# Kernel optimization log

Measured on AMD Instinct MI355X. Metric: run time of the kernel, lower is better.

## Reference

```python
import jax, jax.numpy as jnp
import numpy as np

NEG_INF = -9.0e15  # matches torch's -9000000000000000.0 mask value
ALPHA = 0.2        # LeakyReLU negative slope from init_kwargs


def setup_inputs() -> dict:
    key = jax.random.key(0)
    k1, k2, k3, k4, k5 = jax.random.split(key, 5)
    B, N, D, A = 64, 128, 128, 1000
    hidden = jax.random.normal(k1, (B, N, D), dtype=jnp.float32)
    adj = jax.random.randint(k2, (B, N, N), 0, 5)  # edge types 0..4 (0 = masked)
    a = jax.random.normal(k3, (D, 4), dtype=jnp.float32) * 0.1  # stacked a_0..a_3
    A_attr_sess = jax.random.uniform(k4, (B, N, A), dtype=jnp.float32)
    attr_embedding = jax.random.normal(k5, (A, D), dtype=jnp.float32)
    return {"hidden": hidden, "adj": adj, "a": a,
            "A_attr_sess": A_attr_sess, "attr_embedding": attr_embedding}


def reference(hidden, adj, a, A_attr_sess, attr_embedding):
    # a_input[b,i,j,:] = leaky_relu(h[b,i,:] * h[b,j,:])  -> [B,N,N,D]
    a_input = jax.nn.leaky_relu(hidden[:, :, None, :] * hidden[:, None, :, :],
                                negative_slope=ALPHA)
    # four edge-type scores in one contraction: [B,N,N,4]
    e = jnp.einsum('bijd,dk->bijk', a_input, a)
    # masked selection by adjacency edge type (later writes override earlier)
    alpha = jnp.full(adj.shape, NEG_INF, dtype=e.dtype)
    alpha = jnp.where(adj == 1, e[..., 0], alpha)
    alpha = jnp.where(adj == 2, e[..., 1], alpha)
    alpha = jnp.where(adj == 3, e[..., 2], alpha)
    alpha = jnp.where(adj == 4, e[..., 3], alpha)
    attn = jax.nn.softmax(alpha, axis=-1)        # [B,N,N]
    output = jnp.einsum('bij,bjd->bid', attn, hidden)  # [B,N,D]
    attr_sess = jnp.einsum('bna,ad->bnd', A_attr_sess, attr_embedding)
    return output, attr_sess
```

## Files before the change

kernel.cpp:

```cpp
#include <hip/hip_runtime.h>

#define BB 64
#define NN 128
#define DD 128
#define AA 1000
#define KPAD 1024
#define NEG_INF (-9.0e15f)

typedef __attribute__((ext_vector_type(8))) short short8;
typedef __attribute__((ext_vector_type(4))) float floatx4;
typedef __attribute__((ext_vector_type(4))) unsigned int uintx4;
typedef __attribute__((ext_vector_type(2))) unsigned int uintx2;

__device__ __forceinline__ float bflo(unsigned int u) { return __uint_as_float(u << 16); }
__device__ __forceinline__ float bfhi(unsigned int u) { return __uint_as_float(u & 0xffff0000u); }
__device__ __forceinline__ unsigned int packbf(float f0, float f1) {
  return (__float_as_uint(f0) >> 16) | (__float_as_uint(f1) & 0xffff0000u);
}
__device__ __forceinline__ unsigned short bf_rne(float f) {
  unsigned int u = __float_as_uint(f);
  return (unsigned short)((u + 0x7fffu + ((u >> 16) & 1u)) >> 16);
}
__device__ __forceinline__ unsigned int packbf_rne(float f0, float f1) {
  return (unsigned int)bf_rne(f0) | ((unsigned int)bf_rne(f1) << 16);
}
__device__ __forceinline__ short8 u2s(uintx4 v) {
  union { uintx4 u; short8 s; } x; x.u = v; return x.s;
}

__global__ __launch_bounds__(256) void prep_kernel(
    const float* __restrict__ hidden, const float* __restrict__ emb,
    unsigned short* __restrict__ ET, unsigned short* __restrict__ HTg)
{
  const int t = threadIdx.x;
  const int bid = blockIdx.x;
  if (bid < BB) {
    __shared__ float hsf[NN * 129];
    const float* hb = hidden + (size_t)bid * NN * DD;
    #pragma unroll
    for (int u = 0; u < 16; ++u) {
      int e = u * 1024 + t * 4;
      float4 v = *reinterpret_cast<const float4*>(hb + e);
      int r = e >> 7, c = e & 127;
      float* d = &hsf[r * 129 + c];
      d[0] = v.x; d[1] = v.y; d[2] = v.z; d[3] = v.w;
    }
    __syncthreads();
    unsigned short* ht16 = HTg + (size_t)bid * NN * DD;
    #pragma unroll
    for (int u = 0; u < 8; ++u) {
      int e = u * 2048 + t * 8;
      int dI = e >> 7, il = e & 127;
      float x[8];
      #pragma unroll
      for (int j = 0; j < 8; ++j) x[j] = hsf[(il + j) * 129 + dI];
      uintx4 o;
      o.x = packbf_rne(x[0], x[1]); o.y = packbf_rne(x[2], x[3]);
      o.z = packbf_rne(x[4], x[5]); o.w = packbf_rne(x[6], x[7]);
      *reinterpret_cast<uintx4*>(ht16 + e) = o;
    }
  } else {
    int c = bid - BB;
    int k0 = t * 4;
    float x[4];
    #pragma unroll
    for (int j = 0; j < 4; ++j) {
      int k = k0 + j;
      x[j] = (k < AA) ? emb[(size_t)k * DD + c] : 0.f;
    }
    uintx2 o;
    o.x = packbf_rne(x[0], x[1]);
    o.y = packbf_rne(x[2], x[3]);
    *reinterpret_cast<uintx2*>(ET + (size_t)c * KPAD + k0) = o;
  }
}

struct AttnSmem {
  __align__(16) unsigned short Hs[NN * 128];
  union {
    __align__(16) unsigned short As[4 * 16 * 256];
    struct {
      __align__(16) float Sa[16 * 129];
      __align__(16) unsigned short W[16 * 128];
    } sw;
  } u2;
  __align__(16) float saf[4 * 256];
};

#define BK 64
struct AttrSmem {
  __align__(16) unsigned short ETs[2][DD * BK];
  __align__(16) unsigned short As2[2][32 * BK];
};

union FusedSmem { AttnSmem a; AttrSmem g; };

__device__ __forceinline__ void attn_body(
    AttnSmem& s, const float* __restrict__ hidden,
    const int* __restrict__ adj, const float* __restrict__ amat,
    const unsigned short* __restrict__ HTg, float* __restrict__ out0)
{
  const int t = threadIdx.x;
  const int L = t & 63, w = t >> 6;
  const int lr = L & 15, lq = L >> 4;
  const int b = blockIdx.x >> 3;
  const int i0 = (blockIdx.x & 7) * 16;

  const int* adjb = adj + ((size_t)b * NN + i0) * NN;
  int adjv[8];
  #pragma unroll
  for (int nt = 0; nt < 2; ++nt)
    #pragma unroll
    for (int r = 0; r < 4; ++r)
      adjv[nt * 4 + r] = adjb[(lq * 4 + r) * NN + w * 32 + nt * 16 + lr];

  const float* hb = hidden + (size_t)b * NN * DD;
  #pragma unroll
  for (int u = 0; u < 8; ++u) {
    int id = u * 256 + t;
    int r = id >> 4, c = id & 15;
    const float* src = hb + r * 128 + c * 8;
    float4 v0 = *reinterpret_cast<const float4*>(src);
    float4 v1 = *reinterpret_cast<const float4*>(src + 4);
    uintx4 o;
    o.x = packbf_rne(v0.x, v0.y); o.y = packbf_rne(v0.z, v0.w);
    o.z = packbf_rne(v1.x, v1.y); o.w = packbf_rne(v1.z, v1.w);
    *reinterpret_cast<uintx4*>(&s.Hs[r * 128 + ((c ^ (r & 15)) << 3)]) = o;
  }
  {
    float v1 = amat[t], v2 = amat[t + 256];
    int dI = t >> 2, k = t & 3;
    s.saf[k * 256 + dI] = 0.6f * v1;
    s.saf[k * 256 + 128 + dI] = 0.4f * v1;
    s.saf[k * 256 + 64 + dI] = 0.6f * v2;
    s.saf[k * 256 + 192 + dI] = 0.4f * v2;
  }
  __syncthreads();

  #pragma unroll
  for (int u = 0; u < 8; ++u) {
    int id = u * 256 + t;
    int k = id >> 9, ii = (id >> 5) & 15, c = id & 31;
    int srow = i0 + ii;
    int dchunk = c & 15;
    uintx4 hv = *reinterpret_cast<const uintx4*>(
        &s.Hs[srow * 128 + ((dchunk ^ (srow & 15)) << 3)]);
    if (c & 16) {
      hv.x &= 0x7fff7fffu; hv.y &= 0x7fff7fffu;
      hv.z &= 0x7fff7fffu; hv.w &= 0x7fff7fffu;
    }
    const float* sf = &s.saf[k * 256 + c * 8];
    uintx4 o;
    o.x = packbf(bflo(hv.x) * sf[0], bfhi(hv.x) * sf[1]);
    o.y = packbf(bflo(hv.y) * sf[2], bfhi(hv.y) * sf[3]);
    o.z = packbf(bflo(hv.z) * sf[4], bfhi(hv.z) * sf[5]);
    o.w = packbf(bflo(hv.w) * sf[6], bfhi(hv.w) * sf[7]);
    *reinterpret_cast<uintx4*>(&s.u2.As[k * 4096 + ii * 256 + ((c ^ ii) << 3)]) = o;
  }
  __syncthreads();

  floatx4 acc[4][2];
  #pragma unroll
  for (int k = 0; k < 4; ++k)
    #pragma unroll
    for (int nt = 0; nt < 2; ++nt) acc[k][nt] = floatx4{0.f, 0.f, 0.f, 0.f};

  #pragma unroll
  for (int kt = 0; kt < 8; ++kt) {
    int ca = lq + 4 * kt;
    short8 afr[4];
    #pragma unroll
    for (int k = 0; k < 4; ++k)
      afr[k] = *reinterpret_cast<const short8*>(
          &s.u2.As[k * 4096 + lr * 256 + ((ca ^ lr) << 3)]);
    int cb = lq + 4 * (kt & 3);
    short8 bfr[2];
    #pragma unroll
    for (int nt = 0; nt < 2; ++nt) {
      int jrow = w * 32 + nt * 16 + lr;
      uintx4 hv = *reinterpret_cast<const uintx4*>(
          &s.Hs[jrow * 128 + ((cb ^ (jrow & 15)) << 3)]);
      if (kt >= 4) {
        hv.x &= 0x7fff7fffu; hv.y &= 0x7fff7fffu;
        hv.z &= 0x7fff7fffu; hv.w &= 0x7fff7fffu;
      }
      bfr[nt] = u2s(hv);
    }
    #pragma unroll
    for (int k = 0; k < 4; ++k)
      #pragma unroll
      for (int nt = 0; nt < 2; ++nt)
        acc[k][nt] = __builtin_amdgcn_mfma_f32_16x16x32_bf16(
            afr[k], bfr[nt], acc[k][nt], 0, 0, 0);
  }
  __syncthreads();

  short8 pvb[2][4];
  const unsigned short* ht = HTg + (size_t)b * NN * DD;
  #pragma unroll
  for (int nt = 0; nt < 2; ++nt)
    #pragma unroll
    for (int kt = 0; kt < 4; ++kt) {
      int dI = w * 32 + nt * 16 + lr;
      pvb[nt][kt] = *reinterpret_cast<const short8*>(ht + dI * 128 + kt * 32 + lq * 8);
    }

  #pragma unroll
  for (int nt = 0; nt < 2; ++nt)
    #pragma unroll
    for (int r = 0; r < 4; ++r) {
      int ii = lq * 4 + r;
      int j = w * 32 + nt * 16 + lr;
      int ad = adjv[nt * 4 + r];
      float al = NEG_INF;
      al = (ad == 1) ? acc[0][nt][r] : al;
      al = (ad == 2) ? acc[1][nt][r] : al;
      al = (ad == 3) ? acc[2][nt][r] : al;
      al = (ad == 4) ? acc[3][nt][r] : al;
      s.u2.sw.Sa[ii * 129 + j] = al;
    }
  __syncthreads();

  #pragma unroll
  for (int p = 0; p < 4; ++p) {
    int ii = w * 4 + p;
    float a1 = s.u2.sw.Sa[ii * 129 + L];
    float a2 = s.u2.sw.Sa[ii * 129 + 64 + L];
    float m = fmaxf(a1, a2);
    #pragma unroll
    for (int off = 32; off > 0; off >>= 1) m = fmaxf(m, __shfl_xor(m, off, 64));
    float e1 = __expf(fmaxf(a1 - m, -80.f));
    float e2 = __expf(fmaxf(a2 - m, -80.f));
    float ss = e1 + e2;
    #pragma unroll
    for (int off = 32; off > 0; off >>= 1) ss += __shfl_xor(ss, off, 64);
    float inv = 1.f / ss;
    int j2 = L + 64;
    s.u2.sw.W[ii * 128 + (((L >> 3) ^ ii) << 3) + (L & 7)] = bf_rne(e1 * inv);
    s.u2.sw.W[ii * 128 + (((j2 >> 3) ^ ii) << 3) + (j2 & 7)] = bf_rne(e2 * inv);
  }
  __syncthreads();

  floatx4 oacc[2];
  oacc[0] = floatx4{0.f, 0.f, 0.f, 0.f};
  oacc[1] = floatx4{0.f, 0.f, 0.f, 0.f};
  #pragma unroll
  for (int kt = 0; kt < 4; ++kt) {
    int c = lq + 4 * kt;
    short8 wf = *reinterpret_cast<const short8*>(
        &s.u2.sw.W[lr * 128 + ((c ^ lr) << 3)]);
    #pragma unroll
    for (int nt = 0; nt < 2; ++nt)
      oacc[nt] = __builtin_amdgcn_mfma_f32_16x16x32_bf16(
          wf, pvb[nt][kt], oacc[nt], 0, 0, 0);
  }
  float* ob = out0 + ((size_t)b * NN + i0) * DD;
  #pragma unroll
  for (int nt = 0; nt < 2; ++nt)
    #pragma unroll
    for (int r = 0; r < 4; ++r)
      ob[(lq * 4 + r) * DD + w * 32 + nt * 16 + lr] = oacc[nt][r];
}

__device__ __forceinline__ void attr_body(
    AttrSmem& s, const float* __restrict__ Aattr,
    const unsigned short* __restrict__ ET, float* __restrict__ out1)
{
  const int t = threadIdx.x;
  const int L = t & 63, w = t >> 6;
  const int lr = L & 15, lq = L >> 4;
  const int r0 = (blockIdx.x - 512) * 32;

  float4 pa0, pa1;
  uintx4 pe[4];
  const int ar = t >> 3, ak = (t & 7) * 8;
  const int ec = t >> 1, ej0 = (t & 1) * 4;

  auto fetch = [&](int it) {
    int kb = it * BK;
    int k4 = kb + ak;
    float4 z = {0.f, 0.f, 0.f, 0.f};
    pa0 = (k4 < AA) ? *reinterpret_cast<const float4*>(Aattr + (size_t)(r0 + ar) * AA + k4) : z;
    pa1 = (k4 + 4 < AA) ? *reinterpret_cast<const float4*>(Aattr + (size_t)(r0 + ar) * AA + k4 + 4) : z;
    #pragma unroll
    for (int q = 0; q < 4; ++q)
      pe[q] = *reinterpret_cast<const uintx4*>(ET + (size_t)ec * KPAD + kb + (ej0 + q) * 8);
  };
  auto stage = [&](int buf) {
    uintx4 o;
    o.x = packbf(pa0.x, pa0.y); o.y = packbf(pa0.z, pa0.w);
    o.z = packbf(pa1.x, pa1.y); o.w = packbf(pa1.z, pa1.w);
    int ac = t & 7;
    *reinterpret_cast<uintx4*>(&s.As2[buf][ar * BK + ((ac ^ (ar & 7)) << 3)]) = o;
    #pragma unroll
    for (int q = 0; q < 4; ++q)
      *reinterpret_cast<uintx4*>(&s.ETs[buf][ec * BK + (((ej0 + q) ^ (ec & 7)) << 3)]) = pe[q];
  };

  floatx4 acc[2][2];
  #pragma unroll
  for (int mt = 0; mt < 2; ++mt)
    #pragma unroll
    for (int nt = 0; nt < 2; ++nt) acc[mt][nt] = floatx4{0.f, 0.f, 0.f, 0.f};

  fetch(0);
  for (int it = 0; it < 16; ++it) {
    stage(it & 1);
    __syncthreads();
    if (it < 15) fetch(it + 1);
    #pragma unroll
    for (int ks = 0; ks < 2; ++ks) {
      int c = lq + 4 * ks;
      short8 af[2], bf[2];
      #pragma unroll
      for (int mt = 0; mt < 2; ++mt) {
        int row = mt * 16 + lr;
        af[mt] = *reinterpret_cast<const short8*>(
            &s.As2[it & 1][row * BK + ((c ^ (row & 7)) << 3)]);
      }
      #pragma unroll
      for (int nt = 0; nt < 2; ++nt) {
        int n = w * 32 + nt * 16 + lr;
        bf[nt] = *reinterpret_cast<const short8*>(
            &s.ETs[it & 1][n * BK + ((c ^ (n & 7)) << 3)]);
      }
      #pragma unroll
      for (int mt = 0; mt < 2; ++mt)
        #pragma unroll
        for (int nt = 0; nt < 2; ++nt)
          acc[mt][nt] = __builtin_amdgcn_mfma_f32_16x16x32_bf16(
              af[mt], bf[nt], acc[mt][nt], 0, 0, 0);
    }
  }

  float* ob = out1 + (size_t)r0 * DD;
  #pragma unroll
  for (int mt = 0; mt < 2; ++mt)
    #pragma unroll
    for (int nt = 0; nt < 2; ++nt)
      #pragma unroll
      for (int r = 0; r < 4; ++r)
        ob[(mt * 16 + lq * 4 + r) * DD + w * 32 + nt * 16 + lr] = acc[mt][nt][r];
}

__global__ __launch_bounds__(256, 3) void fused_kernel(
    const float* __restrict__ hidden, const int* __restrict__ adj,
    const float* __restrict__ amat, const float* __restrict__ Aattr,
    const unsigned short* __restrict__ ET, const unsigned short* __restrict__ HTg,
    float* __restrict__ out0, float* __restrict__ out1)
{
  __shared__ FusedSmem sm;
  if (blockIdx.x < 512) attn_body(sm.a, hidden, adj, amat, HTg, out0);
  else                  attr_body(sm.g, Aattr, ET, out1);
}

extern "C" void kernel_launch(void* const* d_in, const int* in_sizes, int n_in,
                              void* d_out, int out_size, void* d_ws, size_t ws_size,
                              hipStream_t stream) {
  const float* hidden = (const float*)d_in[0];
  const int*   adj    = (const int*)d_in[1];
  const float* amat   = (const float*)d_in[2];
  const float* Aattr  = (const float*)d_in[3];
  const float* emb    = (const float*)d_in[4];

  float* out0 = (float*)d_out;
  float* out1 = out0 + (size_t)BB * NN * DD;

  unsigned short* ET  = (unsigned short*)d_ws;
  unsigned short* HTg = ET + (size_t)DD * KPAD;

  prep_kernel<<<BB + DD, 256, 0, stream>>>(hidden, emb, ET, HTg);
  fused_kernel<<<768, 256, 0, stream>>>(hidden, adj, amat, Aattr, ET, HTg,
                                        out0, out1);
}
```

Measured before the change: 105.7 us.

## Pair attention and attribute GEMM work per block, coalesce embedding transpose

The fused kernel now launches 512 blocks, and each block does one 16-row attention tile plus one 16-row attribute-GEMM tile. Even and odd blocks run the two phases in opposite order so memory-heavy and compute-heavy phases are mixed across the GPU, and block indices are remapped. The attribute GEMM tile shrinks to 16 rows with an unrolled double buffer, and launch bounds change from 3 to 2 blocks per SM. The embedding transpose in the prep kernel now goes through shared memory with coalesced loads and runs in 32 blocks instead of 128. The cost is less parallelism per block phase and lower occupancy.

Result: no change. 104.4 us, median of 2 (-1.2%).

```diff
diff --git a/kernel.cpp b/kernel.cpp
--- a/kernel.cpp
+++ b/kernel.cpp
@@ -32,10 +32,10 @@
     const float* __restrict__ hidden, const float* __restrict__ emb,
     unsigned short* __restrict__ ET, unsigned short* __restrict__ HTg)
 {
+  __shared__ float hsf[NN * 129];
   const int t = threadIdx.x;
   const int bid = blockIdx.x;
   if (bid < BB) {
-    __shared__ float hsf[NN * 129];
     const float* hb = hidden + (size_t)bid * NN * DD;
     #pragma unroll
     for (int u = 0; u < 16; ++u) {
@@ -60,18 +60,30 @@
       *reinterpret_cast<uintx4*>(ht16 + e) = o;
     }
   } else {
-    int c = bid - BB;
-    int k0 = t * 4;
-    float x[4];
-    #pragma unroll
-    for (int j = 0; j < 4; ++j) {
-      int k = k0 + j;
-      x[j] = (k < AA) ? emb[(size_t)k * DD + c] : 0.f;
-    }
-    uintx2 o;
-    o.x = packbf_rne(x[0], x[1]);
-    o.y = packbf_rne(x[2], x[3]);
-    *reinterpret_cast<uintx2*>(ET + (size_t)c * KPAD + k0) = o;
+    const int k0 = (bid - BB) * 32;
+    #pragma unroll
+    for (int u = 0; u < 4; ++u) {
+      int e = u * 1024 + t * 4;
+      int r = e >> 7, c = e & 127;
+      float4 z = {0.f, 0.f, 0.f, 0.f};
+      float4 v = (k0 + r < AA)
+          ? *reinterpret_cast<const float4*>(emb + (size_t)(k0 + r) * DD + c) : z;
+      float* d = &hsf[r * 129 + c];
+      d[0] = v.x; d[1] = v.y; d[2] = v.z; d[3] = v.w;
+    }
+    __syncthreads();
+    int c = t >> 1, j0 = (t & 1) * 16;
+    float x[16];
+    #pragma unroll
+    for (int j = 0; j < 16; ++j) x[j] = hsf[(j0 + j) * 129 + c];
+    uintx4 o0, o1;
+    o0.x = packbf_rne(x[0], x[1]);  o0.y = packbf_rne(x[2], x[3]);
+    o0.z = packbf_rne(x[4], x[5]);  o0.w = packbf_rne(x[6], x[7]);
+    o1.x = packbf_rne(x[8], x[9]);  o1.y = packbf_rne(x[10], x[11]);
+    o1.z = packbf_rne(x[12], x[13]); o1.w = packbf_rne(x[14], x[15]);
+    unsigned short* dst = ET + (size_t)c * KPAD + k0 + j0;
+    *reinterpret_cast<uintx4*>(dst) = o0;
+    *reinterpret_cast<uintx4*>(dst + 8) = o1;
   }
 }
 
@@ -90,7 +102,7 @@
 #define BK 64
 struct AttrSmem {
   __align__(16) unsigned short ETs[2][DD * BK];
-  __align__(16) unsigned short As2[2][32 * BK];
+  __align__(16) unsigned short As2[2][16 * BK];
 };
 
 union FusedSmem { AttnSmem a; AttrSmem g; };
@@ -98,13 +110,14 @@
 __device__ __forceinline__ void attn_body(
     AttnSmem& s, const float* __restrict__ hidden,
     const int* __restrict__ adj, const float* __restrict__ amat,
-    const unsigned short* __restrict__ HTg, float* __restrict__ out0)
+    const unsigned short* __restrict__ HTg, float* __restrict__ out0,
+    int wid)
 {
   const int t = threadIdx.x;
   const int L = t & 63, w = t >> 6;
   const int lr = L & 15, lq = L >> 4;
-  const int b = blockIdx.x >> 3;
-  const int i0 = (blockIdx.x & 7) * 16;
+  const int b = wid >> 3;
+  const int i0 = (wid & 7) * 16;
 
   const int* adjb = adj + ((size_t)b * NN + i0) * NN;
   int adjv[8];
@@ -264,94 +277,106 @@
 
 __device__ __forceinline__ void attr_body(
     AttrSmem& s, const float* __restrict__ Aattr,
-    const unsigned short* __restrict__ ET, float* __restrict__ out1)
+    const unsigned short* __restrict__ ET, float* __restrict__ out1,
+    int wid)
 {
   const int t = threadIdx.x;
   const int L = t & 63, w = t >> 6;
   const int lr = L & 15, lq = L >> 4;
-  const int r0 = (blockIdx.x - 512) * 32;
-
-  float4 pa0, pa1;
-  uintx4 pe[4];
-  const int ar = t >> 3, ak = (t & 7) * 8;
+  const int r0 = wid * 16;
+
+  const int ar = t >> 4;
+  const int ak = (t & 15) * 4;
   const int ec = t >> 1, ej0 = (t & 1) * 4;
-
-  auto fetch = [&](int it) {
-    int kb = it * BK;
-    int k4 = kb + ak;
-    float4 z = {0.f, 0.f, 0.f, 0.f};
-    pa0 = (k4 < AA) ? *reinterpret_cast<const float4*>(Aattr + (size_t)(r0 + ar) * AA + k4) : z;
-    pa1 = (k4 + 4 < AA) ? *reinterpret_cast<const float4*>(Aattr + (size_t)(r0 + ar) * AA + k4 + 4) : z;
-    #pragma unroll
-    for (int q = 0; q < 4; ++q)
-      pe[q] = *reinterpret_cast<const uintx4*>(ET + (size_t)ec * KPAD + kb + (ej0 + q) * 8);
-  };
-  auto stage = [&](int buf) {
-    uintx4 o;
-    o.x = packbf(pa0.x, pa0.y); o.y = packbf(pa0.z, pa0.w);
-    o.z = packbf(pa1.x, pa1.y); o.w = packbf(pa1.z, pa1.w);
-    int ac = t & 7;
-    *reinterpret_cast<uintx4*>(&s.As2[buf][ar * BK + ((ac ^ (ar & 7)) << 3)]) = o;
-    #pragma unroll
-    for (int q = 0; q < 4; ++q)
-      *reinterpret_cast<uintx4*>(&s.ETs[buf][ec * BK + (((ej0 + q) ^ (ec & 7)) << 3)]) = pe[q];
-  };
-
-  floatx4 acc[2][2];
-  #pragma unroll
-  for (int mt = 0; mt < 2; ++mt)
-    #pragma unroll
-    for (int nt = 0; nt < 2; ++nt) acc[mt][nt] = floatx4{0.f, 0.f, 0.f, 0.f};
-
-  fetch(0);
-  for (int it = 0; it < 16; ++it) {
-    stage(it & 1);
-    __syncthreads();
-    if (it < 15) fetch(it + 1);
-    #pragma unroll
-    for (int ks = 0; ks < 2; ++ks) {
-      int c = lq + 4 * ks;
-      short8 af[2], bf[2];
-      #pragma unroll
-      for (int mt = 0; mt < 2; ++mt) {
-        int row = mt * 16 + lr;
-        af[mt] = *reinterpret_cast<const short8*>(
-            &s.As2[it & 1][row * BK + ((c ^ (row & 7)) << 3)]);
-      }
-      #pragma unroll
-      for (int nt = 0; nt < 2; ++nt) {
-        int n = w * 32 + nt * 16 + lr;
-        bf[nt] = *reinterpret_cast<const short8*>(
-            &s.ETs[it & 1][n * BK + ((c ^ (n & 7)) << 3)]);
-      }
-      #pragma unroll
-      for (int mt = 0; mt < 2; ++mt)
-        #pragma unroll
-        for (int nt = 0; nt < 2; ++nt)
-          acc[mt][nt] = __builtin_amdgcn_mfma_f32_16x16x32_bf16(
-              af[mt], bf[nt], acc[mt][nt], 0, 0, 0);
-    }
-  }
+  const float* arow = Aattr + (size_t)(r0 + ar) * AA;
+  const unsigned short* erow = ET + (size_t)ec * KPAD;
+
+  float4 paA, paB;
+  uintx4 peA[4], peB[4];
+
+#define ATTR_FETCH(PA, PE, IT) do {                                          \
+    int kb = (IT) * BK; int k4 = kb + ak;                                    \
+    float4 z = {0.f, 0.f, 0.f, 0.f};                                        \
+    PA = (k4 < AA) ? *reinterpret_cast<const float4*>(arow + k4) : z;        \
+    _Pragma("unroll")                                                        \
+    for (int q = 0; q < 4; ++q)                                              \
+      PE[q] = *reinterpret_cast<const uintx4*>(erow + kb + (ej0 + q) * 8);   \
+  } while (0)
+
+#define ATTR_STAGE(PA, PE, BUF) do {                                         \
+    uintx2 o; o.x = packbf(PA.x, PA.y); o.y = packbf(PA.z, PA.w);            \
+    int cidx = ak >> 3, half = ak & 7;                                       \
+    *reinterpret_cast<uintx2*>(                                              \
+        &s.As2[BUF][ar * BK + ((cidx ^ (ar & 7)) << 3) + half]) = o;         \
+    _Pragma("unroll")                                                        \
+    for (int q = 0; q < 4; ++q)                                              \
+      *reinterpret_cast<uintx4*>(                                            \
+          &s.ETs[BUF][ec * BK + (((ej0 + q) ^ (ec & 7)) << 3)]) = PE[q];     \
+  } while (0)
+
+#define ATTR_COMPUTE(BUF) do {                                               \
+    _Pragma("unroll")                                                        \
+    for (int ks = 0; ks < 2; ++ks) {                                         \
+      int c = lq + 4 * ks;                                                   \
+      short8 af = *reinterpret_cast<const short8*>(                          \
+          &s.As2[BUF][lr * BK + ((c ^ (lr & 7)) << 3)]);                     \
+      _Pragma("unroll")                                                      \
+      for (int nt = 0; nt < 2; ++nt) {                                       \
+        int n = w * 32 + nt * 16 + lr;                                       \
+        short8 bf = *reinterpret_cast<const short8*>(                        \
+            &s.ETs[BUF][n * BK + ((c ^ (n & 7)) << 3)]);                     \
+        acc[nt] = __builtin_amdgcn_mfma_f32_16x16x32_bf16(                   \
+            af, bf, acc[nt], 0, 0, 0);                                       \
+      }                                                                      \
+    }                                                                        \
+  } while (0)
+
+  floatx4 acc[2];
+  acc[0] = floatx4{0.f, 0.f, 0.f, 0.f};
+  acc[1] = floatx4{0.f, 0.f, 0.f, 0.f};
+
+  ATTR_FETCH(paA, peA, 0);
+  ATTR_FETCH(paB, peB, 1);
+  for (int ith = 0; ith < 8; ++ith) {
+    ATTR_STAGE(paA, peA, 0);
+    __syncthreads();
+    if (ith < 7) ATTR_FETCH(paA, peA, 2 * ith + 2);
+    ATTR_COMPUTE(0);
+    ATTR_STAGE(paB, peB, 1);
+    __syncthreads();
+    if (ith < 7) ATTR_FETCH(paB, peB, 2 * ith + 3);
+    ATTR_COMPUTE(1);
+  }
+#undef ATTR_FETCH
+#undef ATTR_STAGE
+#undef ATTR_COMPUTE
 
   float* ob = out1 + (size_t)r0 * DD;
   #pragma unroll
-  for (int mt = 0; mt < 2; ++mt)
-    #pragma unroll
-    for (int nt = 0; nt < 2; ++nt)
-      #pragma unroll
-      for (int r = 0; r < 4; ++r)
-        ob[(mt * 16 + lq * 4 + r) * DD + w * 32 + nt * 16 + lr] = acc[mt][nt][r];
-}
-
-__global__ __launch_bounds__(256, 3) void fused_kernel(
+  for (int nt = 0; nt < 2; ++nt)
+    #pragma unroll
+    for (int r = 0; r < 4; ++r)
+      ob[(lq * 4 + r) * DD + w * 32 + nt * 16 + lr] = acc[nt][r];
+}
+
+__global__ __launch_bounds__(256, 2) void fused_kernel(
     const float* __restrict__ hidden, const int* __restrict__ adj,
     const float* __restrict__ amat, const float* __restrict__ Aattr,
     const unsigned short* __restrict__ ET, const unsigned short* __restrict__ HTg,
     float* __restrict__ out0, float* __restrict__ out1)
 {
   __shared__ FusedSmem sm;
-  if (blockIdx.x < 512) attn_body(sm.a, hidden, adj, amat, HTg, out0);
-  else                  attr_body(sm.g, Aattr, ET, out1);
+  const int bid = blockIdx.x;
+  const int wid = (bid & 7) * 64 + (bid >> 3);
+  if (wid & 1) {
+    attn_body(sm.a, hidden, adj, amat, HTg, out0, wid);
+    __syncthreads();
+    attr_body(sm.g, Aattr, ET, out1, wid);
+  } else {
+    attr_body(sm.g, Aattr, ET, out1, wid);
+    __syncthreads();
+    attn_body(sm.a, hidden, adj, amat, HTg, out0, wid);
+  }
 }
 
 extern "C" void kernel_launch(void* const* d_in, const int* in_sizes, int n_in,
@@ -369,7 +394,7 @@
   unsigned short* ET  = (unsigned short*)d_ws;
   unsigned short* HTg = ET + (size_t)DD * KPAD;
 
-  prep_kernel<<<BB + DD, 256, 0, stream>>>(hidden, emb, ET, HTg);
-  fused_kernel<<<768, 256, 0, stream>>>(hidden, adj, amat, Aattr, ET, HTg,
+  prep_kernel<<<BB + 32, 256, 0, stream>>>(hidden, emb, ET, HTg);
+  fused_kernel<<<512, 256, 0, stream>>>(hidden, adj, amat, Aattr, ET, HTg,
                                         out0, out1);
 }
```
